# Optimization experiments

Measured on AMD Instinct MI355X. Metric: run time of the kernel, lower is better.

The kernel has to match this reference:

```python
import jax, jax.numpy as jnp
import numpy as np
import math

B = 256        # batch of series
V = 1024       # vocabulary size (Vocabulary not given; modeled as V random words)
SIZE = 1024    # self.size
CELL = 8       # self.cell_size == word length
SEQ = SIZE // CELL   # 128 segments
DMODEL = 768
NHAAR = 8      # int(log2(128)) + 1
THRESH = 0.95


def _pos_emb():
    position = np.arange(SEQ, dtype=np.float32)[:, None]
    div = np.exp(np.arange(0, DMODEL, 2, dtype=np.float32) * (-math.log(10000.0) / DMODEL))
    pe = np.zeros((SEQ, DMODEL), np.float32)
    pe[:, 0::2] = np.sin(position * div)
    pe[:, 1::2] = np.cos(position * div)
    return jnp.asarray(pe)


def setup_inputs() -> dict:
    key = jax.random.key(0)
    k1, k2, k3, k4 = jax.random.split(key, 4)
    return {
        "X": jax.random.normal(k1, (B, SIZE), jnp.float32),
        "vocab": jax.random.normal(k2, (V, CELL), jnp.float32),
        "word_emb": jax.random.normal(k3, (V, DMODEL), jnp.float32),
        "haar_emb": jax.random.normal(k4, (NHAAR, DMODEL), jnp.float32),
        "pos_emb": _pos_emb(),
    }


def _select(corr):
    """Replicates get_sequence's sequential update over vocabulary order.
    Stored best is the SIGNED correlation c (faithful to the original code),
    compared against |c_new|; accept when |c_new| > threshold and best < |c_new|.
    corr: [B, V, S] -> idx [B, S] (int32, -1 = no word selected)."""
    cs = jnp.transpose(corr, (1, 0, 2))  # [V, B, S]

    def step(carry, xs):
        best, idx = carry
        c, i = xs
        a = jnp.abs(c)
        take = (a > THRESH) & (best < a)
        return (jnp.where(take, c, best), jnp.where(take, i, idx)), None

    init = (jnp.full((corr.shape[0], corr.shape[2]), -jnp.inf, corr.dtype),
            jnp.full((corr.shape[0], corr.shape[2]), -1, jnp.int32))
    (_, idx), _ = jax.lax.scan(step, init, (cs, jnp.arange(V, dtype=jnp.int32)))
    return idx


def _haar_details(x):
    """pywt 'haar' detail coeffs: ds[k] = cD_{k+1}, cD = (x_even - x_odd)/sqrt(2)."""
    inv = jnp.float32(1.0 / math.sqrt(2.0))
    a = x
    ds = []
    for _ in range(10):  # log2(1024) levels
        ds.append((a[:, ::2] - a[:, 1::2]) * inv)
        a = (a[:, ::2] + a[:, 1::2]) * inv
    return ds


def reference(X, vocab, word_emb, haar_emb, pos_emb):
    # --- per-segment cross-correlation against every vocabulary word ---
    seg = X.reshape(B, SEQ, CELL)
    seg_c = seg - seg.mean(-1, keepdims=True)
    seg_std = jnp.sqrt((seg_c * seg_c).mean(-1))          # population std, [B,S]
    w_c = vocab - vocab.mean(-1, keepdims=True)
    w_std = jnp.sqrt((w_c * w_c).mean(-1))                # [V]
    cov = jnp.einsum('bsc,vc->bvs', seg_c, w_c) / CELL    # [B,V,S]
    denom = w_std[None, :, None] * seg_std[:, None, :]
    corr = jnp.where(denom == 0, 0.0, cov / jnp.where(denom == 0, 1.0, denom))

    idx = _select(corr)                                   # [B,S]
    mask = (idx >= 0)

    # --- word embedding lookup (zeros where no word passed threshold) ---
    we = word_emb[jnp.clip(idx, 0, V - 1)] * mask[..., None].astype(word_emb.dtype)

    # --- Haar wavelet coefficients, levels cD_10 .. cD_3 (lengths 1..128) ---
    ds = _haar_details(X)
    pos = jnp.arange(SEQ)
    cols = []
    for l in range(NHAAR):                                # haar_coeffs[l] = cD_{10-l}
        gi = (pos * (2 ** l)) // SEQ                      # i // (SEQ / 2**l)
        cols.append(ds[9 - l][:, gi])                     # [B,S]
    hc = jnp.stack(cols, axis=-1) * mask[..., None].astype(X.dtype)  # [B,S,8]
    haar = jnp.einsum('bsh,hd->bsd', hc, haar_emb)        # [B,S,768]

    return we + pos_emb[None] + haar                      # [B,128,768]
```

## Files before the change

kernel.cpp:

```cpp
#include <hip/hip_runtime.h>
#include <math.h>

#define THRESH_ 0.95f

typedef __attribute__((ext_vector_type(8))) short short8v;
typedef __attribute__((ext_vector_type(16))) float f32x16;

__device__ __forceinline__ unsigned short f2bf_rne(float x) {
    unsigned u = __float_as_uint(x);
    u += 0x7fffu + ((u >> 16) & 1u);
    return (unsigned short)(u >> 16);
}

__global__ __launch_bounds__(512, 4) void k12_fused(const float* __restrict__ X,
                                                    const float* __restrict__ vocab,
                                                    const float* __restrict__ word_emb,
                                                    const float* __restrict__ haar_emb,
                                                    const float* __restrict__ pos_emb,
                                                    float* __restrict__ out) {
    __shared__ float4  wcl4[2048];
    __shared__ short8v wcb_lds[1024];
    __shared__ float   wsl[1024];
    __shared__ float   xrow[1024];
    __shared__ float   segf[1024];
    __shared__ short8v segb[128];
    __shared__ float   sstd_l[128];
    __shared__ float   thr_l[128];
    __shared__ float   stb[512];
    __shared__ int     sti[512];
    __shared__ float   stm[512];
    __shared__ float   tree[254];
    __shared__ float   hc_lds[1024];
    __shared__ int     idx_lds[128];

    int t = threadIdx.x;
    int b = blockIdx.x;

    xrow[t] = X[b * 1024 + t];
    xrow[t + 512] = X[b * 1024 + t + 512];
#pragma unroll
    for (int rep = 0; rep < 2; rep++) {
        int v = t + rep * 512;
        const float4* v4 = (const float4*)vocab + v * 2;
        float4 a = v4[0], bb = v4[1];
        float w[8] = {a.x, a.y, a.z, a.w, bb.x, bb.y, bb.z, bb.w};
        float s = 0.f;
#pragma unroll
        for (int c = 0; c < 8; c++) s += w[c];
        float mean = s * 0.125f;
        float ss = 0.f;
        float wcv[8];
#pragma unroll
        for (int c = 0; c < 8; c++) { wcv[c] = w[c] - mean; ss += wcv[c] * wcv[c]; }
        float sd = sqrtf(ss * 0.125f);
        float4 o0 = {wcv[0], wcv[1], wcv[2], wcv[3]};
        float4 o1 = {wcv[4], wcv[5], wcv[6], wcv[7]};
        wcl4[v * 2] = o0;
        wcl4[v * 2 + 1] = o1;
        wsl[v] = sd;
        union { uint4 q; unsigned short u[8]; } pk;
#pragma unroll
        for (int c = 0; c < 8; c++) pk.u[c] = f2bf_rne(wcv[c]);
        ((uint4*)wcb_lds)[v] = pk.q;
    }
    { stb[t] = -INFINITY; sti[t] = -1; stm[t] = 0.f; }
    __syncthreads();

    if (t < 128) {
        float seg[8];
#pragma unroll
        for (int c = 0; c < 8; c++) seg[c] = xrow[t * 8 + c];
        float sum = 0.f;
#pragma unroll
        for (int c = 0; c < 8; c++) sum += seg[c];
        float mean = sum * 0.125f;
        float segc[8];
        float ss = 0.f;
#pragma unroll
        for (int c = 0; c < 8; c++) { segc[c] = seg[c] - mean; ss += segc[c] * segc[c]; }
        float sstd = sqrtf(ss * 0.125f);
        union { short8v v; unsigned short u[8]; } pk;
#pragma unroll
        for (int c = 0; c < 8; c++) { segf[t * 8 + c] = segc[c]; pk.u[c] = f2bf_rne(segc[c]); }
        segb[t] = pk.v;
        sstd_l[t] = sstd;
        thr_l[t] = 7.52f * sstd;
        tree[t] = sum;
    }
    __syncthreads();

    int w = t >> 6, lane = t & 63;
    {
        int sb = w & 3;
        int gp = w >> 2;
        int half = lane >> 5;

        short8v af = {0, 0, 0, 0, 0, 0, 0, 0};
        if (lane < 32) af = segb[sb * 32 + lane];

        float thr_r[16];
#pragma unroll
        for (int i = 0; i < 16; i++) {
            int row = (i & 3) + 8 * (i >> 2) + 4 * half;
            thr_r[i] = thr_l[sb * 32 + row];
        }

        const double MID = 0x1.E66667p-1;
        for (int gg = 0; gg < 2; gg++) {
            int g = gp * 2 + gg;
            for (int j = 0; j < 8; j++) {
                int wb = g * 8 + j;
                short8v bf = {0, 0, 0, 0, 0, 0, 0, 0};
                if (lane < 32) bf = wcb_lds[wb * 32 + lane];
                float wsd_c = wsl[wb * 32 + (lane & 31)];

                f32x16 accz = {0.f, 0.f, 0.f, 0.f, 0.f, 0.f, 0.f, 0.f,
                               0.f, 0.f, 0.f, 0.f, 0.f, 0.f, 0.f, 0.f};
                f32x16 acc = __builtin_amdgcn_mfma_f32_32x32x16_bf16(af, bf, accz, 0, 0, 0);

                bool anyp = false;
#pragma unroll
                for (int i = 0; i < 16; i++) anyp |= (fabsf(acc[i]) > thr_r[i] * wsd_c);

                if (__builtin_expect(anyp, 0)) {
#pragma unroll
                    for (int i = 0; i < 16; i++) {
                        unsigned long long mi = __ballot(fabsf(acc[i]) > thr_r[i] * wsd_c);
                        while (mi) {
                            int src = __builtin_ctzll(mi);
                            mi &= mi - 1;
                            if (lane == src) {
                                int col = src & 31;
                                int seg_r = sb * 32 + (i & 3) + 8 * (i >> 2) + 4 * (src >> 5);
                                int v = wb * 32 + col;
                                float sst = sstd_l[seg_r];
                                float wsd = wsl[v];
                                const float* sc = &segf[seg_r * 8];
                                float4 wa = wcl4[v * 2];
                                float4 wbv = wcl4[v * 2 + 1];
                                float dot = sc[0] * wa.x + sc[1] * wa.y + sc[2] * wa.z + sc[3] * wa.w
                                          + sc[4] * wbv.x + sc[5] * wbv.y + sc[6] * wbv.z + sc[7] * wbv.w;
                                float cov = dot * 0.125f;
                                float denom = wsd * sst;
                                if ((double)fabsf(cov) >= MID * (double)denom) {
                                    float c = (denom == 0.f) ? 0.f : cov / denom;
                                    float a = fabsf(c);
                                    int sidx = g * 128 + seg_r;
                                    stm[sidx] = fmaxf(stm[sidx], a);
                                    if (a > THRESH_ && stb[sidx] < a) { stb[sidx] = c; sti[sidx] = v; }
                                }
                            }
                        }
                    }
                }
            }
        }
    }
    __syncthreads();

    if (t < 64) tree[128 + t] = tree[2 * t] + tree[2 * t + 1];
    __syncthreads();
    if (t < 32) tree[192 + t] = tree[128 + 2 * t] + tree[128 + 2 * t + 1];
    __syncthreads();
    if (t < 16) tree[224 + t] = tree[192 + 2 * t] + tree[192 + 2 * t + 1];
    __syncthreads();
    if (t < 8) tree[240 + t] = tree[224 + 2 * t] + tree[224 + 2 * t + 1];
    __syncthreads();
    if (t < 4) tree[248 + t] = tree[240 + 2 * t] + tree[240 + 2 * t + 1];
    __syncthreads();
    if (t < 2) tree[252 + t] = tree[248 + 2 * t] + tree[248 + 2 * t + 1];
    __syncthreads();

    if (t < 128) {
        float Bb = stb[t];
        int I = sti[t];
#pragma unroll
        for (int p = 1; p < 4; p++) {
            float yb = stb[p * 128 + t];
            int yi = sti[p * 128 + t];
            float ym = stm[p * 128 + t];
            bool take = (yi != -1) && (!(Bb > THRESH_) || (ym > Bb));
            if (take) { Bb = yb; I = yi; }
        }
        float mask = (I >= 0) ? 1.f : 0.f;

        const int base[7] = {252, 248, 240, 224, 192, 128, 0};
        const float scl[7] = {0.03125f, 0.04419417382415922f, 0.0625f,
                              0.08838834764831843f, 0.125f,
                              0.17677669529663687f, 0.25f};
        float hcv[8];
#pragma unroll
        for (int l = 0; l < 7; l++) {
            int j = (t << l) >> 7;
            hcv[l] = scl[l] * (tree[base[l] + 2 * j] - tree[base[l] + 2 * j + 1]);
        }
        float s4a = xrow[t * 8 + 0] + xrow[t * 8 + 1] + xrow[t * 8 + 2] + xrow[t * 8 + 3];
        float s4b = xrow[t * 8 + 4] + xrow[t * 8 + 5] + xrow[t * 8 + 6] + xrow[t * 8 + 7];
        hcv[7] = 0.3535533905932738f * (s4a - s4b);

#pragma unroll
        for (int l = 0; l < 8; l++) hc_lds[t * 8 + l] = hcv[l] * mask;
        idx_lds[t] = I;
    }
    __syncthreads();

    {
        const float4* pos4 = (const float4*)pos_emb;
        const float4* we4 = (const float4*)word_emb;
        const float4* hg = (const float4*)haar_emb;
        float4* out4 = (float4*)out + (size_t)b * 128 * 192;

        for (int k = 0; k < 16; k++) {
            int row = w * 16 + k;
            int iv = idx_lds[row];
            int ivc = iv < 0 ? 0 : iv;
            float msk = iv < 0 ? 0.f : 1.f;
            float4 ha = *(const float4*)&hc_lds[row * 8];
            float4 hb = *(const float4*)&hc_lds[row * 8 + 4];
            float h[8] = {ha.x, ha.y, ha.z, ha.w, hb.x, hb.y, hb.z, hb.w};

            float4 p0 = pos4[row * 192 + lane];
            float4 p1 = pos4[row * 192 + 64 + lane];
            float4 p2 = pos4[row * 192 + 128 + lane];
            float4 w0 = we4[(size_t)ivc * 192 + lane];
            float4 w1 = we4[(size_t)ivc * 192 + 64 + lane];
            float4 w2 = we4[(size_t)ivc * 192 + 128 + lane];

#pragma unroll
            for (int third = 0; third < 3; third++) {
                int c = third * 64 + lane;
                float4 p = third == 0 ? p0 : (third == 1 ? p1 : p2);
                float4 wv = third == 0 ? w0 : (third == 1 ? w1 : w2);
                float4 acc;
                acc.x = fmaf(wv.x, msk, p.x);
                acc.y = fmaf(wv.y, msk, p.y);
                acc.z = fmaf(wv.z, msk, p.z);
                acc.w = fmaf(wv.w, msk, p.w);
#pragma unroll
                for (int l = 0; l < 8; l++) {
                    float4 he = hg[l * 192 + c];
                    acc.x += h[l] * he.x;
                    acc.y += h[l] * he.y;
                    acc.z += h[l] * he.z;
                    acc.w += h[l] * he.w;
                }
                out4[row * 192 + c] = acc;
            }
        }
    }
}

extern "C" void kernel_launch(void* const* d_in, const int* in_sizes, int n_in,
                              void* d_out, int out_size, void* d_ws, size_t ws_size,
                              hipStream_t stream) {
    const float* X        = (const float*)d_in[0];
    const float* vocab    = (const float*)d_in[1];
    const float* word_emb = (const float*)d_in[2];
    const float* haar_emb = (const float*)d_in[3];
    const float* pos_emb  = (const float*)d_in[4];
    float* out = (float*)d_out;

    hipLaunchKernelGGL(k12_fused, dim3(256), dim3(512), 0, stream,
                       X, vocab, word_emb, haar_emb, pos_emb, out);
}
```

Before: 40.95 us.

## Split segments into halves and overlap output writes with second-half correlation

New measurement: 34.26 us (median of 2 runs). 16.3% less time.

```diff
diff --git a/kernel.cpp b/kernel.cpp
--- a/kernel.cpp
+++ b/kernel.cpp
@@ -3,6 +3,7 @@
 
 #define THRESH_ 0.95f
 
+typedef float nfloat4 __attribute__((ext_vector_type(4)));
 typedef __attribute__((ext_vector_type(8))) short short8v;
 typedef __attribute__((ext_vector_type(16))) float f32x16;
 
@@ -12,12 +13,12 @@
     return (unsigned short)(u >> 16);
 }
 
-__global__ __launch_bounds__(512, 4) void k12_fused(const float* __restrict__ X,
-                                                    const float* __restrict__ vocab,
-                                                    const float* __restrict__ word_emb,
-                                                    const float* __restrict__ haar_emb,
-                                                    const float* __restrict__ pos_emb,
-                                                    float* __restrict__ out) {
+__global__ __launch_bounds__(1024) void k12_fused(const float* __restrict__ X,
+                                                  const float* __restrict__ vocab,
+                                                  const float* __restrict__ word_emb,
+                                                  const float* __restrict__ haar_emb,
+                                                  const float* __restrict__ pos_emb,
+                                                  float* __restrict__ out) {
     __shared__ float4  wcl4[2048];
     __shared__ short8v wcb_lds[1024];
     __shared__ float   wsl[1024];
@@ -26,44 +27,46 @@
     __shared__ short8v segb[128];
     __shared__ float   sstd_l[128];
     __shared__ float   thr_l[128];
-    __shared__ float   stb[512];
-    __shared__ int     sti[512];
-    __shared__ float   stm[512];
+    __shared__ float   stbA[512];
+    __shared__ int     stiA[512];
+    __shared__ float   stmA[512];
+    __shared__ float   stbB[128];
+    __shared__ int     stiB[128];
+    __shared__ float   stmB[128];
     __shared__ float   tree[254];
     __shared__ float   hc_lds[1024];
     __shared__ int     idx_lds[128];
 
     int t = threadIdx.x;
     int b = blockIdx.x;
+    int w = t >> 6, lane = t & 63;
 
     xrow[t] = X[b * 1024 + t];
-    xrow[t + 512] = X[b * 1024 + t + 512];
-#pragma unroll
-    for (int rep = 0; rep < 2; rep++) {
-        int v = t + rep * 512;
-        const float4* v4 = (const float4*)vocab + v * 2;
+    {
+        const float4* v4 = (const float4*)vocab + t * 2;
         float4 a = v4[0], bb = v4[1];
-        float w[8] = {a.x, a.y, a.z, a.w, bb.x, bb.y, bb.z, bb.w};
+        float wv[8] = {a.x, a.y, a.z, a.w, bb.x, bb.y, bb.z, bb.w};
         float s = 0.f;
 #pragma unroll
-        for (int c = 0; c < 8; c++) s += w[c];
+        for (int c = 0; c < 8; c++) s += wv[c];
         float mean = s * 0.125f;
         float ss = 0.f;
         float wcv[8];
 #pragma unroll
-        for (int c = 0; c < 8; c++) { wcv[c] = w[c] - mean; ss += wcv[c] * wcv[c]; }
+        for (int c = 0; c < 8; c++) { wcv[c] = wv[c] - mean; ss += wcv[c] * wcv[c]; }
         float sd = sqrtf(ss * 0.125f);
         float4 o0 = {wcv[0], wcv[1], wcv[2], wcv[3]};
         float4 o1 = {wcv[4], wcv[5], wcv[6], wcv[7]};
-        wcl4[v * 2] = o0;
-        wcl4[v * 2 + 1] = o1;
-        wsl[v] = sd;
+        wcl4[t * 2] = o0;
+        wcl4[t * 2 + 1] = o1;
+        wsl[t] = sd;
         union { uint4 q; unsigned short u[8]; } pk;
 #pragma unroll
         for (int c = 0; c < 8; c++) pk.u[c] = f2bf_rne(wcv[c]);
-        ((uint4*)wcb_lds)[v] = pk.q;
-    }
-    { stb[t] = -INFINITY; sti[t] = -1; stm[t] = 0.f; }
+        ((uint4*)wcb_lds)[t] = pk.q;
+    }
+    if (t < 512) { stbA[t] = -INFINITY; stiA[t] = -1; stmA[t] = 0.f; }
+    if (t < 128) { stbB[t] = -INFINITY; stiB[t] = -1; stmB[t] = 0.f; }
     __syncthreads();
 
     if (t < 128) {
@@ -89,11 +92,12 @@
     }
     __syncthreads();
 
-    int w = t >> 6, lane = t & 63;
+    const double MID = 0x1.E66667p-1;
+
     {
-        int sb = w & 3;
-        int gp = w >> 2;
-        int half = lane >> 5;
+        int sb = w & 1;
+        int g = w >> 1;
+        int lh = lane >> 5;
 
         short8v af = {0, 0, 0, 0, 0, 0, 0, 0};
         if (lane < 32) af = segb[sb * 32 + lane];
@@ -101,54 +105,50 @@
         float thr_r[16];
 #pragma unroll
         for (int i = 0; i < 16; i++) {
-            int row = (i & 3) + 8 * (i >> 2) + 4 * half;
+            int row = (i & 3) + 8 * (i >> 2) + 4 * lh;
             thr_r[i] = thr_l[sb * 32 + row];
         }
 
-        const double MID = 0x1.E66667p-1;
-        for (int gg = 0; gg < 2; gg++) {
-            int g = gp * 2 + gg;
-            for (int j = 0; j < 8; j++) {
-                int wb = g * 8 + j;
-                short8v bf = {0, 0, 0, 0, 0, 0, 0, 0};
-                if (lane < 32) bf = wcb_lds[wb * 32 + lane];
-                float wsd_c = wsl[wb * 32 + (lane & 31)];
-
-                f32x16 accz = {0.f, 0.f, 0.f, 0.f, 0.f, 0.f, 0.f, 0.f,
-                               0.f, 0.f, 0.f, 0.f, 0.f, 0.f, 0.f, 0.f};
-                f32x16 acc = __builtin_amdgcn_mfma_f32_32x32x16_bf16(af, bf, accz, 0, 0, 0);
-
-                bool anyp = false;
-#pragma unroll
-                for (int i = 0; i < 16; i++) anyp |= (fabsf(acc[i]) > thr_r[i] * wsd_c);
-
-                if (__builtin_expect(anyp, 0)) {
-#pragma unroll
-                    for (int i = 0; i < 16; i++) {
-                        unsigned long long mi = __ballot(fabsf(acc[i]) > thr_r[i] * wsd_c);
-                        while (mi) {
-                            int src = __builtin_ctzll(mi);
-                            mi &= mi - 1;
-                            if (lane == src) {
-                                int col = src & 31;
-                                int seg_r = sb * 32 + (i & 3) + 8 * (i >> 2) + 4 * (src >> 5);
-                                int v = wb * 32 + col;
-                                float sst = sstd_l[seg_r];
-                                float wsd = wsl[v];
-                                const float* sc = &segf[seg_r * 8];
-                                float4 wa = wcl4[v * 2];
-                                float4 wbv = wcl4[v * 2 + 1];
-                                float dot = sc[0] * wa.x + sc[1] * wa.y + sc[2] * wa.z + sc[3] * wa.w
-                                          + sc[4] * wbv.x + sc[5] * wbv.y + sc[6] * wbv.z + sc[7] * wbv.w;
-                                float cov = dot * 0.125f;
-                                float denom = wsd * sst;
-                                if ((double)fabsf(cov) >= MID * (double)denom) {
-                                    float c = (denom == 0.f) ? 0.f : cov / denom;
-                                    float a = fabsf(c);
-                                    int sidx = g * 128 + seg_r;
-                                    stm[sidx] = fmaxf(stm[sidx], a);
-                                    if (a > THRESH_ && stb[sidx] < a) { stb[sidx] = c; sti[sidx] = v; }
-                                }
+        for (int j = 0; j < 4; j++) {
+            int wb = g * 4 + j;
+            short8v bf = {0, 0, 0, 0, 0, 0, 0, 0};
+            if (lane < 32) bf = wcb_lds[wb * 32 + lane];
+            float wsd_c = wsl[wb * 32 + (lane & 31)];
+
+            f32x16 accz = {0.f, 0.f, 0.f, 0.f, 0.f, 0.f, 0.f, 0.f,
+                           0.f, 0.f, 0.f, 0.f, 0.f, 0.f, 0.f, 0.f};
+            f32x16 acc = __builtin_amdgcn_mfma_f32_32x32x16_bf16(af, bf, accz, 0, 0, 0);
+
+            bool anyp = false;
+#pragma unroll
+            for (int i = 0; i < 16; i++) anyp |= (fabsf(acc[i]) > thr_r[i] * wsd_c);
+
+            if (__builtin_expect(anyp, 0)) {
+#pragma unroll
+                for (int i = 0; i < 16; i++) {
+                    unsigned long long mi = __ballot(fabsf(acc[i]) > thr_r[i] * wsd_c);
+                    while (mi) {
+                        int src = __builtin_ctzll(mi);
+                        mi &= mi - 1;
+                        if (lane == src) {
+                            int col = src & 31;
+                            int seg_l = sb * 32 + (i & 3) + 8 * (i >> 2) + 4 * (src >> 5);
+                            int v = wb * 32 + col;
+                            float sst = sstd_l[seg_l];
+                            float wsd = wsl[v];
+                            const float* sc = &segf[seg_l * 8];
+                            float4 wa = wcl4[v * 2];
+                            float4 wbv = wcl4[v * 2 + 1];
+                            float dot = sc[0] * wa.x + sc[1] * wa.y + sc[2] * wa.z + sc[3] * wa.w
+                                      + sc[4] * wbv.x + sc[5] * wbv.y + sc[6] * wbv.z + sc[7] * wbv.w;
+                            float cov = dot * 0.125f;
+                            float denom = wsd * sst;
+                            if ((double)fabsf(cov) >= MID * (double)denom) {
+                                float c = (denom == 0.f) ? 0.f : cov / denom;
+                                float a = fabsf(c);
+                                int sidx = g * 64 + seg_l;
+                                stmA[sidx] = fmaxf(stmA[sidx], a);
+                                if (a > THRESH_ && stbA[sidx] < a) { stbA[sidx] = c; stiA[sidx] = v; }
                             }
                         }
                     }
@@ -171,19 +171,20 @@
     if (t < 2) tree[252 + t] = tree[248 + 2 * t] + tree[248 + 2 * t + 1];
     __syncthreads();
 
-    if (t < 128) {
-        float Bb = stb[t];
-        int I = sti[t];
-#pragma unroll
-        for (int p = 1; p < 4; p++) {
-            float yb = stb[p * 128 + t];
-            int yi = sti[p * 128 + t];
-            float ym = stm[p * 128 + t];
+    if (t < 64) {
+        float Bb = stbA[t];
+        int I = stiA[t];
+#pragma unroll
+        for (int p = 1; p < 8; p++) {
+            float yb = stbA[p * 64 + t];
+            int yi = stiA[p * 64 + t];
+            float ym = stmA[p * 64 + t];
             bool take = (yi != -1) && (!(Bb > THRESH_) || (ym > Bb));
             if (take) { Bb = yb; I = yi; }
         }
         float mask = (I >= 0) ? 1.f : 0.f;
 
+        int sg = t;
         const int base[7] = {252, 248, 240, 224, 192, 128, 0};
         const float scl[7] = {0.03125f, 0.04419417382415922f, 0.0625f,
                               0.08838834764831843f, 0.125f,
@@ -191,61 +192,197 @@
         float hcv[8];
 #pragma unroll
         for (int l = 0; l < 7; l++) {
-            int j = (t << l) >> 7;
+            int j = (sg << l) >> 7;
             hcv[l] = scl[l] * (tree[base[l] + 2 * j] - tree[base[l] + 2 * j + 1]);
         }
-        float s4a = xrow[t * 8 + 0] + xrow[t * 8 + 1] + xrow[t * 8 + 2] + xrow[t * 8 + 3];
-        float s4b = xrow[t * 8 + 4] + xrow[t * 8 + 5] + xrow[t * 8 + 6] + xrow[t * 8 + 7];
+        float s4a = xrow[sg * 8 + 0] + xrow[sg * 8 + 1] + xrow[sg * 8 + 2] + xrow[sg * 8 + 3];
+        float s4b = xrow[sg * 8 + 4] + xrow[sg * 8 + 5] + xrow[sg * 8 + 6] + xrow[sg * 8 + 7];
         hcv[7] = 0.3535533905932738f * (s4a - s4b);
 
 #pragma unroll
-        for (int l = 0; l < 8; l++) hc_lds[t * 8 + l] = hcv[l] * mask;
-        idx_lds[t] = I;
-    }
-    __syncthreads();
-
-    {
+        for (int l = 0; l < 8; l++) hc_lds[sg * 8 + l] = hcv[l] * mask;
+        idx_lds[sg] = I;
+    }
+    __syncthreads();
+
+    if (w < 12) {
+        int third = w % 3;
+        int grp = w / 3;
+        int c = third * 64 + lane;
+
+        float4 he[8];
+        const float4* hg = (const float4*)haar_emb;
+#pragma unroll
+        for (int l = 0; l < 8; l++) he[l] = hg[l * 192 + c];
+
         const float4* pos4 = (const float4*)pos_emb;
         const float4* we4 = (const float4*)word_emb;
-        const float4* hg = (const float4*)haar_emb;
         float4* out4 = (float4*)out + (size_t)b * 128 * 192;
 
         for (int k = 0; k < 16; k++) {
-            int row = w * 16 + k;
+            int row = grp * 16 + k;
             int iv = idx_lds[row];
             int ivc = iv < 0 ? 0 : iv;
             float msk = iv < 0 ? 0.f : 1.f;
+            float4 p = pos4[row * 192 + c];
+            float4 wv = we4[(size_t)ivc * 192 + c];
             float4 ha = *(const float4*)&hc_lds[row * 8];
             float4 hb = *(const float4*)&hc_lds[row * 8 + 4];
             float h[8] = {ha.x, ha.y, ha.z, ha.w, hb.x, hb.y, hb.z, hb.w};
 
-            float4 p0 = pos4[row * 192 + lane];
-            float4 p1 = pos4[row * 192 + 64 + lane];
-            float4 p2 = pos4[row * 192 + 128 + lane];
-            float4 w0 = we4[(size_t)ivc * 192 + lane];
-            float4 w1 = we4[(size_t)ivc * 192 + 64 + lane];
-            float4 w2 = we4[(size_t)ivc * 192 + 128 + lane];
-
-#pragma unroll
-            for (int third = 0; third < 3; third++) {
-                int c = third * 64 + lane;
-                float4 p = third == 0 ? p0 : (third == 1 ? p1 : p2);
-                float4 wv = third == 0 ? w0 : (third == 1 ? w1 : w2);
-                float4 acc;
-                acc.x = fmaf(wv.x, msk, p.x);
-                acc.y = fmaf(wv.y, msk, p.y);
-                acc.z = fmaf(wv.z, msk, p.z);
-                acc.w = fmaf(wv.w, msk, p.w);
-#pragma unroll
-                for (int l = 0; l < 8; l++) {
-                    float4 he = hg[l * 192 + c];
-                    acc.x += h[l] * he.x;
-                    acc.y += h[l] * he.y;
-                    acc.z += h[l] * he.z;
-                    acc.w += h[l] * he.w;
+            float4 acc;
+            acc.x = fmaf(wv.x, msk, p.x);
+            acc.y = fmaf(wv.y, msk, p.y);
+            acc.z = fmaf(wv.z, msk, p.z);
+            acc.w = fmaf(wv.w, msk, p.w);
+#pragma unroll
+            for (int l = 0; l < 8; l++) {
+                acc.x += h[l] * he[l].x;
+                acc.y += h[l] * he[l].y;
+                acc.z += h[l] * he[l].z;
+                acc.w += h[l] * he[l].w;
+            }
+            nfloat4 nv = {acc.x, acc.y, acc.z, acc.w};
+            __builtin_nontemporal_store(nv, (nfloat4*)&out4[row * 192 + c]);
+        }
+    } else {
+        int wl = w - 12;
+        int sb = wl & 1;
+        int g = wl >> 1;
+        int lh = lane >> 5;
+
+        short8v af = {0, 0, 0, 0, 0, 0, 0, 0};
+        if (lane < 32) af = segb[64 + sb * 32 + lane];
+
+        float thr_r[16];
+#pragma unroll
+        for (int i = 0; i < 16; i++) {
+            int row = (i & 3) + 8 * (i >> 2) + 4 * lh;
+            thr_r[i] = thr_l[64 + sb * 32 + row];
+        }
+
+        for (int j = 0; j < 16; j++) {
+            int wb = g * 16 + j;
+            short8v bf = {0, 0, 0, 0, 0, 0, 0, 0};
+            if (lane < 32) bf = wcb_lds[wb * 32 + lane];
+            float wsd_c = wsl[wb * 32 + (lane & 31)];
+
+            f32x16 accz = {0.f, 0.f, 0.f, 0.f, 0.f, 0.f, 0.f, 0.f,
+                           0.f, 0.f, 0.f, 0.f, 0.f, 0.f, 0.f, 0.f};
+            f32x16 acc = __builtin_amdgcn_mfma_f32_32x32x16_bf16(af, bf, accz, 0, 0, 0);
+
+            bool anyp = false;
+#pragma unroll
+            for (int i = 0; i < 16; i++) anyp |= (fabsf(acc[i]) > thr_r[i] * wsd_c);
+
+            if (__builtin_expect(anyp, 0)) {
+#pragma unroll
+                for (int i = 0; i < 16; i++) {
+                    unsigned long long mi = __ballot(fabsf(acc[i]) > thr_r[i] * wsd_c);
+                    while (mi) {
+                        int src = __builtin_ctzll(mi);
+                        mi &= mi - 1;
+                        if (lane == src) {
+                            int col = src & 31;
+                            int seg_l = sb * 32 + (i & 3) + 8 * (i >> 2) + 4 * (src >> 5);
+                            int sg = 64 + seg_l;
+                            int v = wb * 32 + col;
+                            float sst = sstd_l[sg];
+                            float wsd = wsl[v];
+                            const float* sc = &segf[sg * 8];
+                            float4 wa = wcl4[v * 2];
+                            float4 wbv = wcl4[v * 2 + 1];
+                            float dot = sc[0] * wa.x + sc[1] * wa.y + sc[2] * wa.z + sc[3] * wa.w
+                                      + sc[4] * wbv.x + sc[5] * wbv.y + sc[6] * wbv.z + sc[7] * wbv.w;
+                            float cov = dot * 0.125f;
+                            float denom = wsd * sst;
+                            if ((double)fabsf(cov) >= MID * (double)denom) {
+                                float c = (denom == 0.f) ? 0.f : cov / denom;
+                                float a = fabsf(c);
+                                int sidx = g * 64 + seg_l;
+                                stmB[sidx] = fmaxf(stmB[sidx], a);
+                                if (a > THRESH_ && stbB[sidx] < a) { stbB[sidx] = c; stiB[sidx] = v; }
+                            }
+                        }
+                    }
                 }
-                out4[row * 192 + c] = acc;
             }
+        }
+    }
+    __syncthreads();
+
+    if (t < 64) {
+        float Bb = stbB[t];
+        int I = stiB[t];
+        {
+            float yb = stbB[64 + t];
+            int yi = stiB[64 + t];
+            float ym = stmB[64 + t];
+            bool take = (yi != -1) && (!(Bb > THRESH_) || (ym > Bb));
+            if (take) { Bb = yb; I = yi; }
+        }
+        float mask = (I >= 0) ? 1.f : 0.f;
+
+        int sg = 64 + t;
+        const int base[7] = {252, 248, 240, 224, 192, 128, 0};
+        const float scl[7] = {0.03125f, 0.04419417382415922f, 0.0625f,
+                              0.08838834764831843f, 0.125f,
+                              0.17677669529663687f, 0.25f};
+        float hcv[8];
+#pragma unroll
+        for (int l = 0; l < 7; l++) {
+            int j = (sg << l) >> 7;
+            hcv[l] = scl[l] * (tree[base[l] + 2 * j] - tree[base[l] + 2 * j + 1]);
+        }
+        float s4a = xrow[sg * 8 + 0] + xrow[sg * 8 + 1] + xrow[sg * 8 + 2] + xrow[sg * 8 + 3];
+        float s4b = xrow[sg * 8 + 4] + xrow[sg * 8 + 5] + xrow[sg * 8 + 6] + xrow[sg * 8 + 7];
+        hcv[7] = 0.3535533905932738f * (s4a - s4b);
+
+#pragma unroll
+        for (int l = 0; l < 8; l++) hc_lds[sg * 8 + l] = hcv[l] * mask;
+        idx_lds[sg] = I;
+    }
+    __syncthreads();
+
+    if (w < 12) {
+        int third = w % 3;
+        int grp = w / 3;
+        int c = third * 64 + lane;
+
+        float4 he[8];
+        const float4* hg = (const float4*)haar_emb;
+#pragma unroll
+        for (int l = 0; l < 8; l++) he[l] = hg[l * 192 + c];
+
+        const float4* pos4 = (const float4*)pos_emb;
+        const float4* we4 = (const float4*)word_emb;
+        float4* out4 = (float4*)out + (size_t)b * 128 * 192;
+
+        for (int k = 0; k < 16; k++) {
+            int row = 64 + grp * 16 + k;
+            int iv = idx_lds[row];
+            int ivc = iv < 0 ? 0 : iv;
+            float msk = iv < 0 ? 0.f : 1.f;
+            float4 p = pos4[row * 192 + c];
+            float4 wv = we4[(size_t)ivc * 192 + c];
+            float4 ha = *(const float4*)&hc_lds[row * 8];
+            float4 hb = *(const float4*)&hc_lds[row * 8 + 4];
+            float h[8] = {ha.x, ha.y, ha.z, ha.w, hb.x, hb.y, hb.z, hb.w};
+
+            float4 acc;
+            acc.x = fmaf(wv.x, msk, p.x);
+            acc.y = fmaf(wv.y, msk, p.y);
+            acc.z = fmaf(wv.z, msk, p.z);
+            acc.w = fmaf(wv.w, msk, p.w);
+#pragma unroll
+            for (int l = 0; l < 8; l++) {
+                acc.x += h[l] * he[l].x;
+                acc.y += h[l] * he[l].y;
+                acc.z += h[l] * he[l].z;
+                acc.w += h[l] * he[l].w;
+            }
+            nfloat4 nv = {acc.x, acc.y, acc.z, acc.w};
+            __builtin_nontemporal_store(nv, (nfloat4*)&out4[row * 192 + c]);
         }
     }
 }
@@ -260,6 +397,6 @@
     const float* pos_emb  = (const float*)d_in[4];
     float* out = (float*)d_out;
 
-    hipLaunchKernelGGL(k12_fused, dim3(256), dim3(512), 0, stream,
+    hipLaunchKernelGGL(k12_fused, dim3(256), dim3(1024), 0, stream,
                        X, vocab, word_emb, haar_emb, pos_emb, out);
 }
```

## Specialize waves into producer and consumer roles with LDS flag handoff

Applied to the files above, without the earlier changes.

New measurement: 40.96 us. No clear change (+0.0%).

```diff
diff --git a/kernel.cpp b/kernel.cpp
--- a/kernel.cpp
+++ b/kernel.cpp
@@ -3,6 +3,7 @@
 
 #define THRESH_ 0.95f
 
+typedef float nfloat4 __attribute__((ext_vector_type(4)));
 typedef __attribute__((ext_vector_type(8))) short short8v;
 typedef __attribute__((ext_vector_type(16))) float f32x16;
 
@@ -12,12 +13,12 @@
     return (unsigned short)(u >> 16);
 }
 
-__global__ __launch_bounds__(512, 4) void k12_fused(const float* __restrict__ X,
-                                                    const float* __restrict__ vocab,
-                                                    const float* __restrict__ word_emb,
-                                                    const float* __restrict__ haar_emb,
-                                                    const float* __restrict__ pos_emb,
-                                                    float* __restrict__ out) {
+__global__ __launch_bounds__(1024) void k12_fused(const float* __restrict__ X,
+                                                  const float* __restrict__ vocab,
+                                                  const float* __restrict__ word_emb,
+                                                  const float* __restrict__ haar_emb,
+                                                  const float* __restrict__ pos_emb,
+                                                  float* __restrict__ out) {
     __shared__ float4  wcl4[2048];
     __shared__ short8v wcb_lds[1024];
     __shared__ float   wsl[1024];
@@ -26,44 +27,43 @@
     __shared__ short8v segb[128];
     __shared__ float   sstd_l[128];
     __shared__ float   thr_l[128];
-    __shared__ float   stb[512];
-    __shared__ int     sti[512];
-    __shared__ float   stm[512];
+    __shared__ float   stb[128];
+    __shared__ int     sti[128];
     __shared__ float   tree[254];
     __shared__ float   hc_lds[1024];
     __shared__ int     idx_lds[128];
+    __shared__ int     flags[4];
 
     int t = threadIdx.x;
     int b = blockIdx.x;
+    int w = t >> 6, lane = t & 63;
 
     xrow[t] = X[b * 1024 + t];
-    xrow[t + 512] = X[b * 1024 + t + 512];
-#pragma unroll
-    for (int rep = 0; rep < 2; rep++) {
-        int v = t + rep * 512;
-        const float4* v4 = (const float4*)vocab + v * 2;
+    {
+        const float4* v4 = (const float4*)vocab + t * 2;
         float4 a = v4[0], bb = v4[1];
-        float w[8] = {a.x, a.y, a.z, a.w, bb.x, bb.y, bb.z, bb.w};
+        float wv[8] = {a.x, a.y, a.z, a.w, bb.x, bb.y, bb.z, bb.w};
         float s = 0.f;
 #pragma unroll
-        for (int c = 0; c < 8; c++) s += w[c];
+        for (int c = 0; c < 8; c++) s += wv[c];
         float mean = s * 0.125f;
         float ss = 0.f;
         float wcv[8];
 #pragma unroll
-        for (int c = 0; c < 8; c++) { wcv[c] = w[c] - mean; ss += wcv[c] * wcv[c]; }
+        for (int c = 0; c < 8; c++) { wcv[c] = wv[c] - mean; ss += wcv[c] * wcv[c]; }
         float sd = sqrtf(ss * 0.125f);
         float4 o0 = {wcv[0], wcv[1], wcv[2], wcv[3]};
         float4 o1 = {wcv[4], wcv[5], wcv[6], wcv[7]};
-        wcl4[v * 2] = o0;
-        wcl4[v * 2 + 1] = o1;
-        wsl[v] = sd;
+        wcl4[t * 2] = o0;
+        wcl4[t * 2 + 1] = o1;
+        wsl[t] = sd;
         union { uint4 q; unsigned short u[8]; } pk;
 #pragma unroll
         for (int c = 0; c < 8; c++) pk.u[c] = f2bf_rne(wcv[c]);
-        ((uint4*)wcb_lds)[v] = pk.q;
+        ((uint4*)wcb_lds)[t] = pk.q;
     }
-    { stb[t] = -INFINITY; sti[t] = -1; stm[t] = 0.f; }
+    if (t < 128) { stb[t] = -INFINITY; sti[t] = -1; }
+    if (t < 4) flags[t] = 0;
     __syncthreads();
 
     if (t < 128) {
@@ -89,163 +89,144 @@
     }
     __syncthreads();
 
-    int w = t >> 6, lane = t & 63;
-    {
-        int sb = w & 3;
-        int gp = w >> 2;
-        int half = lane >> 5;
+    if (t < 64) tree[128 + t] = tree[2 * t] + tree[2 * t + 1];
+    __syncthreads();
+    if (t < 32) tree[192 + t] = tree[128 + 2 * t] + tree[128 + 2 * t + 1];
+    __syncthreads();
+    if (t < 16) tree[224 + t] = tree[192 + 2 * t] + tree[192 + 2 * t + 1];
+    __syncthreads();
+    if (t < 8) tree[240 + t] = tree[224 + 2 * t] + tree[224 + 2 * t + 1];
+    __syncthreads();
+    if (t < 4) tree[248 + t] = tree[240 + 2 * t] + tree[240 + 2 * t + 1];
+    __syncthreads();
+    if (t < 2) tree[252 + t] = tree[248 + 2 * t] + tree[248 + 2 * t + 1];
+    __syncthreads();
+
+    const double MID = 0x1.E66667p-1;
+
+    if (w < 4) {
+        int lh = lane >> 5;
 
         short8v af = {0, 0, 0, 0, 0, 0, 0, 0};
-        if (lane < 32) af = segb[sb * 32 + lane];
+        if (lane < 32) af = segb[w * 32 + lane];
 
         float thr_r[16];
 #pragma unroll
         for (int i = 0; i < 16; i++) {
-            int row = (i & 3) + 8 * (i >> 2) + 4 * half;
-            thr_r[i] = thr_l[sb * 32 + row];
-        }
-
-        const double MID = 0x1.E66667p-1;
-        for (int gg = 0; gg < 2; gg++) {
-            int g = gp * 2 + gg;
-            for (int j = 0; j < 8; j++) {
-                int wb = g * 8 + j;
-                short8v bf = {0, 0, 0, 0, 0, 0, 0, 0};
-                if (lane < 32) bf = wcb_lds[wb * 32 + lane];
-                float wsd_c = wsl[wb * 32 + (lane & 31)];
-
-                f32x16 accz = {0.f, 0.f, 0.f, 0.f, 0.f, 0.f, 0.f, 0.f,
-                               0.f, 0.f, 0.f, 0.f, 0.f, 0.f, 0.f, 0.f};
-                f32x16 acc = __builtin_amdgcn_mfma_f32_32x32x16_bf16(af, bf, accz, 0, 0, 0);
-
-                bool anyp = false;
-#pragma unroll
-                for (int i = 0; i < 16; i++) anyp |= (fabsf(acc[i]) > thr_r[i] * wsd_c);
-
-                if (__builtin_expect(anyp, 0)) {
-#pragma unroll
-                    for (int i = 0; i < 16; i++) {
-                        unsigned long long mi = __ballot(fabsf(acc[i]) > thr_r[i] * wsd_c);
-                        while (mi) {
-                            int src = __builtin_ctzll(mi);
-                            mi &= mi - 1;
-                            if (lane == src) {
-                                int col = src & 31;
-                                int seg_r = sb * 32 + (i & 3) + 8 * (i >> 2) + 4 * (src >> 5);
-                                int v = wb * 32 + col;
-                                float sst = sstd_l[seg_r];
-                                float wsd = wsl[v];
-                                const float* sc = &segf[seg_r * 8];
-                                float4 wa = wcl4[v * 2];
-                                float4 wbv = wcl4[v * 2 + 1];
-                                float dot = sc[0] * wa.x + sc[1] * wa.y + sc[2] * wa.z + sc[3] * wa.w
-                                          + sc[4] * wbv.x + sc[5] * wbv.y + sc[6] * wbv.z + sc[7] * wbv.w;
-                                float cov = dot * 0.125f;
-                                float denom = wsd * sst;
-                                if ((double)fabsf(cov) >= MID * (double)denom) {
-                                    float c = (denom == 0.f) ? 0.f : cov / denom;
-                                    float a = fabsf(c);
-                                    int sidx = g * 128 + seg_r;
-                                    stm[sidx] = fmaxf(stm[sidx], a);
-                                    if (a > THRESH_ && stb[sidx] < a) { stb[sidx] = c; sti[sidx] = v; }
-                                }
+            int row = (i & 3) + 8 * (i >> 2) + 4 * lh;
+            thr_r[i] = thr_l[w * 32 + row];
+        }
+
+        for (int wb = 0; wb < 32; wb++) {
+            short8v bf = {0, 0, 0, 0, 0, 0, 0, 0};
+            if (lane < 32) bf = wcb_lds[wb * 32 + lane];
+            float wsd_c = wsl[wb * 32 + (lane & 31)];
+
+            f32x16 accz = {0.f, 0.f, 0.f, 0.f, 0.f, 0.f, 0.f, 0.f,
+                           0.f, 0.f, 0.f, 0.f, 0.f, 0.f, 0.f, 0.f};
+            f32x16 acc = __builtin_amdgcn_mfma_f32_32x32x16_bf16(af, bf, accz, 0, 0, 0);
+
+            bool anyp = false;
+#pragma unroll
+            for (int i = 0; i < 16; i++) anyp |= (fabsf(acc[i]) > thr_r[i] * wsd_c);
+
+            if (__builtin_expect(anyp, 0)) {
+#pragma unroll
+                for (int i = 0; i < 16; i++) {
+                    unsigned long long mi = __ballot(fabsf(acc[i]) > thr_r[i] * wsd_c);
+                    while (mi) {
+                        int src = __builtin_ctzll(mi);
+                        mi &= mi - 1;
+                        if (lane == src) {
+                            int col = src & 31;
+                            int sg = w * 32 + (i & 3) + 8 * (i >> 2) + 4 * (src >> 5);
+                            int v = wb * 32 + col;
+                            float sst = sstd_l[sg];
+                            float wsd = wsl[v];
+                            const float* sc = &segf[sg * 8];
+                            float4 wa = wcl4[v * 2];
+                            float4 wbv = wcl4[v * 2 + 1];
+                            float dot = sc[0] * wa.x + sc[1] * wa.y + sc[2] * wa.z + sc[3] * wa.w
+                                      + sc[4] * wbv.x + sc[5] * wbv.y + sc[6] * wbv.z + sc[7] * wbv.w;
+                            float cov = dot * 0.125f;
+                            float denom = wsd * sst;
+                            if ((double)fabsf(cov) >= MID * (double)denom) {
+                                float c = (denom == 0.f) ? 0.f : cov / denom;
+                                float a = fabsf(c);
+                                if (a > THRESH_ && stb[sg] < a) { stb[sg] = c; sti[sg] = v; }
                             }
                         }
                     }
                 }
             }
         }
-    }
-    __syncthreads();
-
-    if (t < 64) tree[128 + t] = tree[2 * t] + tree[2 * t + 1];
-    __syncthreads();
-    if (t < 32) tree[192 + t] = tree[128 + 2 * t] + tree[128 + 2 * t + 1];
-    __syncthreads();
-    if (t < 16) tree[224 + t] = tree[192 + 2 * t] + tree[192 + 2 * t + 1];
-    __syncthreads();
-    if (t < 8) tree[240 + t] = tree[224 + 2 * t] + tree[224 + 2 * t + 1];
-    __syncthreads();
-    if (t < 4) tree[248 + t] = tree[240 + 2 * t] + tree[240 + 2 * t + 1];
-    __syncthreads();
-    if (t < 2) tree[252 + t] = tree[248 + 2 * t] + tree[248 + 2 * t + 1];
-    __syncthreads();
-
-    if (t < 128) {
-        float Bb = stb[t];
-        int I = sti[t];
-#pragma unroll
-        for (int p = 1; p < 4; p++) {
-            float yb = stb[p * 128 + t];
-            int yi = sti[p * 128 + t];
-            float ym = stm[p * 128 + t];
-            bool take = (yi != -1) && (!(Bb > THRESH_) || (ym > Bb));
-            if (take) { Bb = yb; I = yi; }
-        }
-        float mask = (I >= 0) ? 1.f : 0.f;
-
-        const int base[7] = {252, 248, 240, 224, 192, 128, 0};
-        const float scl[7] = {0.03125f, 0.04419417382415922f, 0.0625f,
-                              0.08838834764831843f, 0.125f,
-                              0.17677669529663687f, 0.25f};
-        float hcv[8];
-#pragma unroll
-        for (int l = 0; l < 7; l++) {
-            int j = (t << l) >> 7;
-            hcv[l] = scl[l] * (tree[base[l] + 2 * j] - tree[base[l] + 2 * j + 1]);
-        }
-        float s4a = xrow[t * 8 + 0] + xrow[t * 8 + 1] + xrow[t * 8 + 2] + xrow[t * 8 + 3];
-        float s4b = xrow[t * 8 + 4] + xrow[t * 8 + 5] + xrow[t * 8 + 6] + xrow[t * 8 + 7];
-        hcv[7] = 0.3535533905932738f * (s4a - s4b);
-
-#pragma unroll
-        for (int l = 0; l < 8; l++) hc_lds[t * 8 + l] = hcv[l] * mask;
-        idx_lds[t] = I;
-    }
-    __syncthreads();
-
-    {
+
+        if (lane < 32) {
+            int sg = w * 32 + lane;
+            int I = sti[sg];
+            float mask = (I >= 0) ? 1.f : 0.f;
+
+            const int base[7] = {252, 248, 240, 224, 192, 128, 0};
+            const float scl[7] = {0.03125f, 0.04419417382415922f, 0.0625f,
+                                  0.08838834764831843f, 0.125f,
+                                  0.17677669529663687f, 0.25f};
+            float hcv[8];
+#pragma unroll
+            for (int l = 0; l < 7; l++) {
+                int j = (sg << l) >> 7;
+                hcv[l] = scl[l] * (tree[base[l] + 2 * j] - tree[base[l] + 2 * j + 1]);
+            }
+            float s4a = xrow[sg * 8 + 0] + xrow[sg * 8 + 1] + xrow[sg * 8 + 2] + xrow[sg * 8 + 3];
+            float s4b = xrow[sg * 8 + 4] + xrow[sg * 8 + 5] + xrow[sg * 8 + 6] + xrow[sg * 8 + 7];
+            hcv[7] = 0.3535533905932738f * (s4a - s4b);
+
+#pragma unroll
+            for (int l = 0; l < 8; l++) hc_lds[sg * 8 + l] = hcv[l] * mask;
+            idx_lds[sg] = I;
+        }
+        __hip_atomic_store(&flags[w], 1, __ATOMIC_RELEASE, __HIP_MEMORY_SCOPE_WORKGROUP);
+    } else {
+        int q = (w - 4) / 3;
+        int third = (w - 4) % 3;
+        int c = third * 64 + lane;
+
+        float4 he[8];
+        const float4* hg = (const float4*)haar_emb;
+#pragma unroll
+        for (int l = 0; l < 8; l++) he[l] = hg[l * 192 + c];
+
+        while (__hip_atomic_load(&flags[q], __ATOMIC_ACQUIRE, __HIP_MEMORY_SCOPE_WORKGROUP) == 0)
+            __builtin_amdgcn_s_sleep(2);
+
         const float4* pos4 = (const float4*)pos_emb;
         const float4* we4 = (const float4*)word_emb;
-        const float4* hg = (const float4*)haar_emb;
         float4* out4 = (float4*)out + (size_t)b * 128 * 192;
 
-        for (int k = 0; k < 16; k++) {
-            int row = w * 16 + k;
+        for (int k = 0; k < 32; k++) {
+            int row = q * 32 + k;
             int iv = idx_lds[row];
             int ivc = iv < 0 ? 0 : iv;
             float msk = iv < 0 ? 0.f : 1.f;
+            float4 p = pos4[row * 192 + c];
+            float4 wv = we4[(size_t)ivc * 192 + c];
             float4 ha = *(const float4*)&hc_lds[row * 8];
             float4 hb = *(const float4*)&hc_lds[row * 8 + 4];
             float h[8] = {ha.x, ha.y, ha.z, ha.w, hb.x, hb.y, hb.z, hb.w};
 
-            float4 p0 = pos4[row * 192 + lane];
-            float4 p1 = pos4[row * 192 + 64 + lane];
-            float4 p2 = pos4[row * 192 + 128 + lane];
-            float4 w0 = we4[(size_t)ivc * 192 + lane];
-            float4 w1 = we4[(size_t)ivc * 192 + 64 + lane];
-            float4 w2 = we4[(size_t)ivc * 192 + 128 + lane];
-
-#pragma unroll
-            for (int third = 0; third < 3; third++) {
-                int c = third * 64 + lane;
-                float4 p = third == 0 ? p0 : (third == 1 ? p1 : p2);
-                float4 wv = third == 0 ? w0 : (third == 1 ? w1 : w2);
-                float4 acc;
-                acc.x = fmaf(wv.x, msk, p.x);
-                acc.y = fmaf(wv.y, msk, p.y);
-                acc.z = fmaf(wv.z, msk, p.z);
-                acc.w = fmaf(wv.w, msk, p.w);
-#pragma unroll
-                for (int l = 0; l < 8; l++) {
-                    float4 he = hg[l * 192 + c];
-                    acc.x += h[l] * he.x;
-                    acc.y += h[l] * he.y;
-                    acc.z += h[l] * he.z;
-                    acc.w += h[l] * he.w;
-                }
-                out4[row * 192 + c] = acc;
+            float4 acc;
+            acc.x = fmaf(wv.x, msk, p.x);
+            acc.y = fmaf(wv.y, msk, p.y);
+            acc.z = fmaf(wv.z, msk, p.z);
+            acc.w = fmaf(wv.w, msk, p.w);
+#pragma unroll
+            for (int l = 0; l < 8; l++) {
+                acc.x += h[l] * he[l].x;
+                acc.y += h[l] * he[l].y;
+                acc.z += h[l] * he[l].z;
+                acc.w += h[l] * he[l].w;
             }
+            nfloat4 nv = {acc.x, acc.y, acc.z, acc.w};
+            __builtin_nontemporal_store(nv, (nfloat4*)&out4[row * 192 + c]);
         }
     }
 }
@@ -260,6 +241,6 @@
     const float* pos_emb  = (const float*)d_in[4];
     float* out = (float*)d_out;
 
-    hipLaunchKernelGGL(k12_fused, dim3(256), dim3(512), 0, stream,
+    hipLaunchKernelGGL(k12_fused, dim3(256), dim3(1024), 0, stream,
                        X, vocab, word_emb, haar_emb, pos_emb, out);
 }
```

## Split fused kernel into selection kernel and wide output-writing kernel

Applied to the files above, without the earlier changes.

After: 42.01 us. +2.6%, slower.

```diff
diff --git a/kernel.cpp b/kernel.cpp
--- a/kernel.cpp
+++ b/kernel.cpp
@@ -12,12 +12,11 @@
     return (unsigned short)(u >> 16);
 }
 
-__global__ __launch_bounds__(512, 4) void k12_fused(const float* __restrict__ X,
-                                                    const float* __restrict__ vocab,
-                                                    const float* __restrict__ word_emb,
-                                                    const float* __restrict__ haar_emb,
-                                                    const float* __restrict__ pos_emb,
-                                                    float* __restrict__ out) {
+
+__global__ __launch_bounds__(1024) void kA_select(const float* __restrict__ X,
+                                                  const float* __restrict__ vocab,
+                                                  float* __restrict__ hcw,
+                                                  int* __restrict__ idxw) {
     __shared__ float4  wcl4[2048];
     __shared__ short8v wcb_lds[1024];
     __shared__ float   wsl[1024];
@@ -30,18 +29,13 @@
     __shared__ int     sti[512];
     __shared__ float   stm[512];
     __shared__ float   tree[254];
-    __shared__ float   hc_lds[1024];
-    __shared__ int     idx_lds[128];
 
     int t = threadIdx.x;
     int b = blockIdx.x;
 
     xrow[t] = X[b * 1024 + t];
-    xrow[t + 512] = X[b * 1024 + t + 512];
-#pragma unroll
-    for (int rep = 0; rep < 2; rep++) {
-        int v = t + rep * 512;
-        const float4* v4 = (const float4*)vocab + v * 2;
+    {
+        const float4* v4 = (const float4*)vocab + t * 2;
         float4 a = v4[0], bb = v4[1];
         float w[8] = {a.x, a.y, a.z, a.w, bb.x, bb.y, bb.z, bb.w};
         float s = 0.f;
@@ -55,15 +49,15 @@
         float sd = sqrtf(ss * 0.125f);
         float4 o0 = {wcv[0], wcv[1], wcv[2], wcv[3]};
         float4 o1 = {wcv[4], wcv[5], wcv[6], wcv[7]};
-        wcl4[v * 2] = o0;
-        wcl4[v * 2 + 1] = o1;
-        wsl[v] = sd;
+        wcl4[t * 2] = o0;
+        wcl4[t * 2 + 1] = o1;
+        wsl[t] = sd;
         union { uint4 q; unsigned short u[8]; } pk;
 #pragma unroll
         for (int c = 0; c < 8; c++) pk.u[c] = f2bf_rne(wcv[c]);
-        ((uint4*)wcb_lds)[v] = pk.q;
-    }
-    { stb[t] = -INFINITY; sti[t] = -1; stm[t] = 0.f; }
+        ((uint4*)wcb_lds)[t] = pk.q;
+    }
+    if (t < 512) { stb[t] = -INFINITY; sti[t] = -1; stm[t] = 0.f; }
     __syncthreads();
 
     if (t < 128) {
@@ -92,7 +86,7 @@
     int w = t >> 6, lane = t & 63;
     {
         int sb = w & 3;
-        int gp = w >> 2;
+        int g = w >> 2;
         int half = lane >> 5;
 
         short8v af = {0, 0, 0, 0, 0, 0, 0, 0};
@@ -106,49 +100,46 @@
         }
 
         const double MID = 0x1.E66667p-1;
-        for (int gg = 0; gg < 2; gg++) {
-            int g = gp * 2 + gg;
-            for (int j = 0; j < 8; j++) {
-                int wb = g * 8 + j;
-                short8v bf = {0, 0, 0, 0, 0, 0, 0, 0};
-                if (lane < 32) bf = wcb_lds[wb * 32 + lane];
-                float wsd_c = wsl[wb * 32 + (lane & 31)];
-
-                f32x16 accz = {0.f, 0.f, 0.f, 0.f, 0.f, 0.f, 0.f, 0.f,
-                               0.f, 0.f, 0.f, 0.f, 0.f, 0.f, 0.f, 0.f};
-                f32x16 acc = __builtin_amdgcn_mfma_f32_32x32x16_bf16(af, bf, accz, 0, 0, 0);
-
-                bool anyp = false;
-#pragma unroll
-                for (int i = 0; i < 16; i++) anyp |= (fabsf(acc[i]) > thr_r[i] * wsd_c);
-
-                if (__builtin_expect(anyp, 0)) {
-#pragma unroll
-                    for (int i = 0; i < 16; i++) {
-                        unsigned long long mi = __ballot(fabsf(acc[i]) > thr_r[i] * wsd_c);
-                        while (mi) {
-                            int src = __builtin_ctzll(mi);
-                            mi &= mi - 1;
-                            if (lane == src) {
-                                int col = src & 31;
-                                int seg_r = sb * 32 + (i & 3) + 8 * (i >> 2) + 4 * (src >> 5);
-                                int v = wb * 32 + col;
-                                float sst = sstd_l[seg_r];
-                                float wsd = wsl[v];
-                                const float* sc = &segf[seg_r * 8];
-                                float4 wa = wcl4[v * 2];
-                                float4 wbv = wcl4[v * 2 + 1];
-                                float dot = sc[0] * wa.x + sc[1] * wa.y + sc[2] * wa.z + sc[3] * wa.w
-                                          + sc[4] * wbv.x + sc[5] * wbv.y + sc[6] * wbv.z + sc[7] * wbv.w;
-                                float cov = dot * 0.125f;
-                                float denom = wsd * sst;
-                                if ((double)fabsf(cov) >= MID * (double)denom) {
-                                    float c = (denom == 0.f) ? 0.f : cov / denom;
-                                    float a = fabsf(c);
-                                    int sidx = g * 128 + seg_r;
-                                    stm[sidx] = fmaxf(stm[sidx], a);
-                                    if (a > THRESH_ && stb[sidx] < a) { stb[sidx] = c; sti[sidx] = v; }
-                                }
+        for (int j = 0; j < 8; j++) {
+            int wb = g * 8 + j;
+            short8v bf = {0, 0, 0, 0, 0, 0, 0, 0};
+            if (lane < 32) bf = wcb_lds[wb * 32 + lane];
+            float wsd_c = wsl[wb * 32 + (lane & 31)];
+
+            f32x16 accz = {0.f, 0.f, 0.f, 0.f, 0.f, 0.f, 0.f, 0.f,
+                           0.f, 0.f, 0.f, 0.f, 0.f, 0.f, 0.f, 0.f};
+            f32x16 acc = __builtin_amdgcn_mfma_f32_32x32x16_bf16(af, bf, accz, 0, 0, 0);
+
+            bool anyp = false;
+#pragma unroll
+            for (int i = 0; i < 16; i++) anyp |= (fabsf(acc[i]) > thr_r[i] * wsd_c);
+
+            if (__builtin_expect(anyp, 0)) {
+#pragma unroll
+                for (int i = 0; i < 16; i++) {
+                    unsigned long long mi = __ballot(fabsf(acc[i]) > thr_r[i] * wsd_c);
+                    while (mi) {
+                        int src = __builtin_ctzll(mi);
+                        mi &= mi - 1;
+                        if (lane == src) {
+                            int col = src & 31;
+                            int seg_r = sb * 32 + (i & 3) + 8 * (i >> 2) + 4 * (src >> 5);
+                            int v = wb * 32 + col;
+                            float sst = sstd_l[seg_r];
+                            float wsd = wsl[v];
+                            const float* sc = &segf[seg_r * 8];
+                            float4 wa = wcl4[v * 2];
+                            float4 wbv = wcl4[v * 2 + 1];
+                            float dot = sc[0] * wa.x + sc[1] * wa.y + sc[2] * wa.z + sc[3] * wa.w
+                                      + sc[4] * wbv.x + sc[5] * wbv.y + sc[6] * wbv.z + sc[7] * wbv.w;
+                            float cov = dot * 0.125f;
+                            float denom = wsd * sst;
+                            if ((double)fabsf(cov) >= MID * (double)denom) {
+                                float c = (denom == 0.f) ? 0.f : cov / denom;
+                                float a = fabsf(c);
+                                int sidx = g * 128 + seg_r;
+                                stm[sidx] = fmaxf(stm[sidx], a);
+                                if (a > THRESH_ && stb[sidx] < a) { stb[sidx] = c; sti[sidx] = v; }
                             }
                         }
                     }
@@ -198,53 +189,66 @@
         float s4b = xrow[t * 8 + 4] + xrow[t * 8 + 5] + xrow[t * 8 + 6] + xrow[t * 8 + 7];
         hcv[7] = 0.3535533905932738f * (s4a - s4b);
 
-#pragma unroll
-        for (int l = 0; l < 8; l++) hc_lds[t * 8 + l] = hcv[l] * mask;
-        idx_lds[t] = I;
-    }
-    __syncthreads();
-
-    {
-        const float4* pos4 = (const float4*)pos_emb;
-        const float4* we4 = (const float4*)word_emb;
-        const float4* hg = (const float4*)haar_emb;
-        float4* out4 = (float4*)out + (size_t)b * 128 * 192;
-
-        for (int k = 0; k < 16; k++) {
-            int row = w * 16 + k;
-            int iv = idx_lds[row];
-            int ivc = iv < 0 ? 0 : iv;
-            float msk = iv < 0 ? 0.f : 1.f;
-            float4 ha = *(const float4*)&hc_lds[row * 8];
-            float4 hb = *(const float4*)&hc_lds[row * 8 + 4];
-            float h[8] = {ha.x, ha.y, ha.z, ha.w, hb.x, hb.y, hb.z, hb.w};
-
-            float4 p0 = pos4[row * 192 + lane];
-            float4 p1 = pos4[row * 192 + 64 + lane];
-            float4 p2 = pos4[row * 192 + 128 + lane];
-            float4 w0 = we4[(size_t)ivc * 192 + lane];
-            float4 w1 = we4[(size_t)ivc * 192 + 64 + lane];
-            float4 w2 = we4[(size_t)ivc * 192 + 128 + lane];
-
-#pragma unroll
-            for (int third = 0; third < 3; third++) {
-                int c = third * 64 + lane;
-                float4 p = third == 0 ? p0 : (third == 1 ? p1 : p2);
-                float4 wv = third == 0 ? w0 : (third == 1 ? w1 : w2);
+        int row = b * 128 + t;
+        float4 o0 = {hcv[0] * mask, hcv[1] * mask, hcv[2] * mask, hcv[3] * mask};
+        float4 o1 = {hcv[4] * mask, hcv[5] * mask, hcv[6] * mask, hcv[7] * mask};
+        ((float4*)hcw)[row * 2] = o0;
+        ((float4*)hcw)[row * 2 + 1] = o1;
+        idxw[row] = I;
+    }
+}
+
+__global__ __launch_bounds__(256) void kB_out(const float* __restrict__ word_emb,
+                                              const float* __restrict__ haar_emb,
+                                              const float* __restrict__ pos_emb,
+                                              const float* __restrict__ hcw,
+                                              const int* __restrict__ idxw,
+                                              float* __restrict__ out) {
+    int t = threadIdx.x;
+    int lane = t & 63, wave = t >> 6;
+
+    float4 he_r[3][8];
+    const float4* hg = (const float4*)haar_emb;
+#pragma unroll
+    for (int cb = 0; cb < 3; cb++)
+#pragma unroll
+        for (int l = 0; l < 8; l++)
+            he_r[cb][l] = hg[l * 192 + cb * 64 + lane];
+
+    int rbase = (int)blockIdx.x * 32 + wave * 8;
+    for (int k = 0; k < 8; k++) {
+        int r = rbase + k;
+        int iv = idxw[r];
+        int s = r & 127;
+        const float4* p4 = (const float4*)pos_emb + s * 192;
+        float4* o4 = (float4*)out + (size_t)r * 192;
+        if (iv >= 0) {
+            float h[8];
+#pragma unroll
+            for (int l = 0; l < 8; l++) h[l] = hcw[r * 8 + l];
+            const float4* w4 = (const float4*)word_emb + iv * 192;
+#pragma unroll
+            for (int cb = 0; cb < 3; cb++) {
+                int c = cb * 64 + lane;
+                float4 p = p4[c];
+                float4 w = w4[c];
                 float4 acc;
-                acc.x = fmaf(wv.x, msk, p.x);
-                acc.y = fmaf(wv.y, msk, p.y);
-                acc.z = fmaf(wv.z, msk, p.z);
-                acc.w = fmaf(wv.w, msk, p.w);
+                acc.x = p.x + w.x; acc.y = p.y + w.y;
+                acc.z = p.z + w.z; acc.w = p.w + w.w;
 #pragma unroll
                 for (int l = 0; l < 8; l++) {
-                    float4 he = hg[l * 192 + c];
-                    acc.x += h[l] * he.x;
-                    acc.y += h[l] * he.y;
-                    acc.z += h[l] * he.z;
-                    acc.w += h[l] * he.w;
+                    acc.x += h[l] * he_r[cb][l].x;
+                    acc.y += h[l] * he_r[cb][l].y;
+                    acc.z += h[l] * he_r[cb][l].z;
+                    acc.w += h[l] * he_r[cb][l].w;
                 }
-                out4[row * 192 + c] = acc;
+                o4[c] = acc;
+            }
+        } else {
+#pragma unroll
+            for (int cb = 0; cb < 3; cb++) {
+                int c = cb * 64 + lane;
+                o4[c] = p4[c];
             }
         }
     }
@@ -260,6 +264,11 @@
     const float* pos_emb  = (const float*)d_in[4];
     float* out = (float*)d_out;
 
-    hipLaunchKernelGGL(k12_fused, dim3(256), dim3(512), 0, stream,
-                       X, vocab, word_emb, haar_emb, pos_emb, out);
-}
+    float* wsf  = (float*)d_ws;
+    float* hcw  = wsf;
+    int*   idxw = (int*)(wsf + 262144);
+
+    hipLaunchKernelGGL(kA_select, dim3(256), dim3(1024), 0, stream, X, vocab, hcw, idxw);
+    hipLaunchKernelGGL(kB_out, dim3(1024), dim3(256), 0, stream,
+                       word_emb, haar_emb, pos_emb, hcw, idxw, out);
+}
```
